# Performance work log

Hardware: AMD Instinct MI355X
Metric: run time of the kernel (lower is better)

The kernel has to match this reference:

```python
import jax, jax.numpy as jnp
import numpy as np

EPS = 1e-08


def setup_inputs() -> dict:
    key = jax.random.key(0)
    k1, k2, k3 = jax.random.split(key, 3)
    b, c, s = 4, 128, 32
    oc, k = 128, 3
    x = jax.random.normal(k1, (b, c, s, s, s), dtype=jnp.float32)
    y = jax.random.normal(k2, (b, c), dtype=jnp.float32)
    weight = jax.random.normal(k3, (oc, c, k, k, k), dtype=jnp.float32)
    return {"x": x, "y": y, "weight": weight}


def reference(x, y, weight):
    b, c, h, w, d = x.shape
    oc, ic, kh, kw, kd = weight.shape
    # modulate: per-sample scale of input channels
    ws = weight[None] * y[:, None, :, None, None, None]  # (b, oc, ic, k, k, k)
    # demodulate
    demod = jax.lax.rsqrt(jnp.sum(jnp.square(ws), axis=(2, 3, 4, 5)) + EPS)  # (b, oc)
    ws = ws * demod[:, :, None, None, None, None]
    # grouped conv: fold batch into channels, groups=b
    xr = x.reshape(1, b * c, h, w, d)
    wr = ws.reshape(b * oc, ic, kh, kw, kd)
    # same padding for stride=1, dilation=1: (k-1)//2
    pad = (kh - 1) // 2
    out = jax.lax.conv_general_dilated(
        xr, wr,
        window_strides=(1, 1, 1),
        padding=[(pad, pad)] * 3,
        feature_group_count=b,
        dimension_numbers=("NCDHW", "OIDHW", "NCDHW"),
    )
    return out.reshape(b, oc, h, w, d)
```

## Files before the change

### kernel.cpp

```cpp
#include <hip/hip_runtime.h>
#include <hip/hip_bf16.h>

typedef __attribute__((ext_vector_type(8))) short bf16x8;
typedef __attribute__((ext_vector_type(4))) float f32x4;
typedef unsigned short u16;
typedef unsigned int u32;

#define NP 34
#define XT_BYTES ((size_t)4 * NP * NP * NP * 128 * 2)

__device__ __forceinline__ u16 f2bf(float f) {
  __hip_bfloat16 h = __float2bfloat16(f);
  return __builtin_bit_cast(u16, h);
}

__device__ __forceinline__ void gload_lds16(const u16* g, u16* l) {
  __builtin_amdgcn_global_load_lds(
      (const __attribute__((address_space(1))) u32*)g,
      (__attribute__((address_space(3))) u32*)l, 16, 0, 0);
}

#define WAITV(N) asm volatile("s_waitcnt vmcnt(" #N ")" ::: "memory")
#define BAR() do { __builtin_amdgcn_s_barrier(); asm volatile("" ::: "memory"); } while (0)

__global__ __launch_bounds__(128) void kmodw(const float* __restrict__ w,
                                             const float* __restrict__ y,
                                             u16* __restrict__ wmod) {
  const int oc = blockIdx.x, b = blockIdx.y;
  const int ic = threadIdx.x;
  const float* wp = w + (oc * 128 + ic) * 27;
  float wv[27];
  float s = 0.f;
#pragma unroll
  for (int t = 0; t < 27; ++t) { wv[t] = wp[t]; s += wv[t] * wv[t]; }
  const float yv = y[b * 128 + ic];
  float v = yv * yv * s;
#pragma unroll
  for (int m = 1; m < 64; m <<= 1) v += __shfl_xor(v, m);
  __shared__ float part[2];
  const int lane = ic & 63, wid = ic >> 6;
  if (lane == 0) part[wid] = v;
  __syncthreads();
  const float demod = rsqrtf(part[0] + part[1] + 1e-8f);
  const float sc = yv * demod;
#pragma unroll
  for (int t = 0; t < 27; ++t)
    wmod[((b * 27 + t) * 128 + oc) * 128 + ic] = f2bf(wv[t] * sc);
}

__global__ __launch_bounds__(128) void khalo(u16* __restrict__ xt) {
  const int zy = blockIdx.x, b = blockIdx.y;
  const int zz = zy / NP, yy = zy % NP;
  u16* row = xt + ((size_t)((b * NP + zz) * NP + yy) * NP) * 128;
  u32* wp = (u32*)row;
  if (zz == 0 || zz == NP - 1 || yy == 0 || yy == NP - 1) {
#pragma unroll
    for (int i = 0; i < 17; ++i) wp[i * 128 + threadIdx.x] = 0;
  } else {
    if (threadIdx.x < 64) wp[threadIdx.x] = 0;
    else ((u32*)(row + 33 * 128))[threadIdx.x - 64] = 0;
  }
}

__global__ __launch_bounds__(256) void kcastx(const float* __restrict__ x,
                                              u16* __restrict__ xt) {
  const int yq = blockIdx.x, z = blockIdx.y, b = blockIdx.z;
  const int tid = threadIdx.x;
  __shared__ u16 t[32 * 132];
  const float* xp = x + (size_t)b * 128 * 32768 + (z * 32 + yq) * 32;
#pragma unroll
  for (int p = 0; p < 16; ++p) {
    const int ic = p * 8 + (tid >> 5), xx = tid & 31;
    t[xx * 132 + ic] = f2bf(xp[(size_t)ic * 32768 + xx]);
  }
  __syncthreads();
  u16* xtb = xt + (((size_t)(b * NP + z + 1) * NP + (yq + 1)) * NP + 1) * 128;
#pragma unroll
  for (int p = 0; p < 4; ++p) {
    const int xx = p * 8 + (tid >> 5), icq = tid & 31;
    *(ushort4*)(xtb + (size_t)xx * 128 + icq * 4) = *(const ushort4*)&t[xx * 132 + icq * 4];
  }
}

__global__ __launch_bounds__(512, 2) void kconv(const u16* __restrict__ xt,
                                                const u16* __restrict__ wmod,
                                                float* __restrict__ out) {
  __shared__ __align__(16) u16 Bsm[40960];
  __shared__ __align__(16) u16 Asm[3][8192];
  const int tid = threadIdx.x;
  const int lane = tid & 63, wn = tid >> 6;
  const int l15 = lane & 15, sgq = lane >> 4;
  const int bid = blockIdx.x;
  const int wgid = ((bid & 7) << 5) + (bid >> 3);
  const int b = wgid >> 6, yt = (wgid >> 5) & 1, z = wgid & 31;
  const int y0 = yt << 4;

  const u16* xb = xt + (size_t)b * (NP * NP * NP) * 128;
  const u16* wb = wmod + (size_t)b * 27 * 16384;

  f32x4 acc[8][4];
#pragma unroll
  for (int i = 0; i < 8; ++i)
#pragma unroll
    for (int j = 0; j < 4; ++j) acc[i][j] = (f32x4){0.f, 0.f, 0.f, 0.f};

  const int aoc = tid >> 3, aj = tid & 7;
  const u16* asrc = wb + (aoc << 7) + ((aj ^ (aoc & 7)) << 3);
  const int adst = tid << 3;

  int sybase[4], xp0[4];
#pragma unroll
  for (int nf = 0; nf < 4; ++nf) {
    sybase[nf] = (((wn << 1) + (nf >> 1)) + 1) * 2176;
    xp0[nf] = ((nf & 1) << 4) + l15 + 1;
  }
  const int kswz0 = sgq ^ (l15 & 7);

  auto stageA1 = [&](int ks2, int k) {
    const int g2 = ks2 / 9, j2 = ks2 - g2 * 9;
    const int tap = (g2 >> 1) * 9 + j2, hh = g2 & 1;
    gload_lds16(asrc + tap * 16384 + (hh << 6) + (k << 13),
                &Asm[ks2 % 3][adst + (k << 12)]);
  };
  auto stageB = [&](int g) {
    const int dz = (g >> 1) - 1, hh = g & 1;
    const int zrow = (z + 1 + dz) * NP + y0;
#pragma unroll
    for (int r = 0; r < 10; ++r) {
      int s = r * 512 + tid;
      const int dst = s << 3;
      s = s < 4896 ? s : 4895;
      const int sy = s / 272;
      const int rem = s - sy * 272;
      const int xpos = rem >> 3, j = rem & 7;
      gload_lds16(xb + (size_t)((zrow + sy) * NP + xpos) * 128 + (hh << 6) +
                      ((j ^ (xpos & 7)) << 3),
                  &Bsm[dst]);
    }
  };
  auto ldAf = [&](bf16x8* af, int par, int mh, int kswz) {
    const u16* Ah = &Asm[par][0];
#pragma unroll
    for (int mm = 0; mm < 4; ++mm) {
      const int oc = (mh << 6) + (mm << 4) + l15;
      af[mm] = *(const bf16x8*)&Ah[(oc << 6) + (kswz << 3)];
    }
  };
  auto ldBv = [&](bf16x8* bv, int kk, int dy, int dx) {
#pragma unroll
    for (int nf = 0; nf < 4; ++nf) {
      const int xp = xp0[nf] + dx;
      const int off = sybase[nf] + dy * 2176 + (xp << 6) +
                      ((((kk << 2) + sgq) ^ (xp & 7)) << 3);
      bv[nf] = *(const bf16x8*)&Bsm[off];
    }
  };

  bf16x8 af0[4], af1[4], bv0[4], bv1[4];

#define MFMA16(MH, AF, BV)                                                 \
  { __builtin_amdgcn_s_setprio(1);                                         \
    _Pragma("unroll") for (int mm = 0; mm < 4; ++mm)                       \
      _Pragma("unroll") for (int nf = 0; nf < 4; ++nf)                     \
        acc[(MH) * 4 + mm][nf] = __builtin_amdgcn_mfma_f32_16x16x32_bf16(  \
            (AF)[mm], (BV)[nf], acc[(MH) * 4 + mm][nf], 0, 0, 0);          \
    __builtin_amdgcn_s_setprio(0); }

  stageB(0);
  stageA1(0, 0); stageA1(0, 1);
  stageA1(1, 0); stageA1(1, 1);
  WAITV(0); BAR();

  for (int g = 0; g < 6; ++g) {
    for (int j = 0; j < 9; ++j) {
      const int ks = g * 9 + j;
      const int par = ks % 3;
      const int dy = j / 3 - 1, dx = (j % 3) - 1;
      const int ks2 = (ks + 2 <= 53) ? ks + 2 : 53;
      ldAf(af0, par, 0, kswz0);
      ldBv(bv0, 0, dy, dx);
      stageA1(ks2, 0);
      MFMA16(0, af0, bv0);
      ldAf(af1, par, 1, kswz0);
      stageA1(ks2, 1);
      MFMA16(1, af1, bv0);
      ldAf(af0, par, 0, kswz0 ^ 4);
      ldBv(bv1, 1, dy, dx);
      MFMA16(0, af0, bv1);
      ldAf(af1, par, 1, kswz0 ^ 4);
      MFMA16(1, af1, bv1);
      if (j < 8) {
        WAITV(2); BAR();
      } else if (g < 5) {
        BAR();
        stageB(g + 1);
        WAITV(0); BAR();
      }
    }
  }

#pragma unroll
  for (int m = 0; m < 8; ++m) {
    const int ocb = (m << 4) + (sgq << 2);
#pragma unroll
    for (int nf = 0; nf < 4; ++nf) {
      const int n = (wn << 6) + (nf << 4) + l15;
      const int yy = n >> 5, xx = n & 31;
      float* op = out + ((size_t)(b * 128 + ocb) << 15) + (z << 10) +
                  ((y0 + yy) << 5) + xx;
#pragma unroll
      for (int r = 0; r < 4; ++r) op[(size_t)r << 15] = acc[m][nf][r];
    }
  }
#undef MFMA16
}

extern "C" void kernel_launch(void* const* d_in, const int* in_sizes, int n_in,
                              void* d_out, int out_size, void* d_ws, size_t ws_size,
                              hipStream_t stream) {
  const float* x = (const float*)d_in[0];
  const float* y = (const float*)d_in[1];
  const float* w = (const float*)d_in[2];
  float* out = (float*)d_out;
  u16* xt = (u16*)d_ws;
  u16* wmod = (u16*)((char*)d_ws + XT_BYTES);

  hipLaunchKernelGGL(khalo, dim3(NP * NP, 4), dim3(128), 0, stream, xt);
  hipLaunchKernelGGL(kmodw, dim3(128, 4), dim3(128), 0, stream, w, y, wmod);
  hipLaunchKernelGGL(kcastx, dim3(32, 32, 4), dim3(256), 0, stream, x, xt);
  hipLaunchKernelGGL(kconv, dim3(256), dim3(512), 0, stream, xt, wmod, out);
}
```

Baseline: 122.8 us.

## Halve conv workgroup tile to 8 rows, 256 threads, double-buffered weights

The conv kernel now uses 256-thread workgroups that each cover 8 output rows instead of 16, doubling the grid to 512 blocks. The input slab shrinks to 10 rows, and the weight tile becomes double-buffered, with a full 128x64 slice staged each k-step. The smaller LDS footprint lets two workgroups share a CU, so one can hide the other's barrier stalls. In exchange, weights are reloaded twice as often across the grid, the halo overhead per block rises, and prefetch depth drops from two steps to one with a full vmcnt(0) wait each step.

```diff
diff --git a/kernel.cpp b/kernel.cpp
--- a/kernel.cpp
+++ b/kernel.cpp
@@ -82,21 +82,21 @@
   }
 }
 
-__global__ __launch_bounds__(512, 2) void kconv(const u16* __restrict__ xt,
+__global__ __launch_bounds__(256, 2) void kconv(const u16* __restrict__ xt,
                                                 const u16* __restrict__ wmod,
                                                 float* __restrict__ out) {
-  __shared__ __align__(16) u16 Bsm[40960];
-  __shared__ __align__(16) u16 Asm[3][8192];
+  __shared__ __align__(16) u16 Asm[2][8192];
+  __shared__ __align__(16) u16 Bsm[22528];
   const int tid = threadIdx.x;
   const int lane = tid & 63, wn = tid >> 6;
   const int l15 = lane & 15, sgq = lane >> 4;
   const int bid = blockIdx.x;
-  const int wgid = ((bid & 7) << 5) + (bid >> 3);
-  const int b = wgid >> 6, yt = (wgid >> 5) & 1, z = wgid & 31;
-  const int y0 = yt << 4;
-
+  const int wgid = ((bid & 7) << 6) + (bid >> 3);
+  const int b = wgid >> 7, yt = (wgid >> 5) & 3, z = wgid & 31;
+  const int y0 = yt << 3;
+
+  const u16* wb = wmod + (size_t)b * 27 * 16384;
   const u16* xb = xt + (size_t)b * (NP * NP * NP) * 128;
-  const u16* wb = wmod + (size_t)b * 27 * 16384;
 
   f32x4 acc[8][4];
 #pragma unroll
@@ -104,10 +104,9 @@
 #pragma unroll
     for (int j = 0; j < 4; ++j) acc[i][j] = (f32x4){0.f, 0.f, 0.f, 0.f};
 
-  const int aoc = tid >> 3, aj = tid & 7;
-  const u16* asrc = wb + (aoc << 7) + ((aj ^ (aoc & 7)) << 3);
+  const int aoc0 = tid >> 3, aj = tid & 7;
+  const u16* asrc = wb + (aoc0 << 7) + ((aj ^ (aoc0 & 7)) << 3);
   const int adst = tid << 3;
-
   int sybase[4], xp0[4];
 #pragma unroll
   for (int nf = 0; nf < 4; ++nf) {
@@ -116,24 +115,27 @@
   }
   const int kswz0 = sgq ^ (l15 & 7);
 
-  auto stageA1 = [&](int ks2, int k) {
-    const int g2 = ks2 / 9, j2 = ks2 - g2 * 9;
-    const int tap = (g2 >> 1) * 9 + j2, hh = g2 & 1;
-    gload_lds16(asrc + tap * 16384 + (hh << 6) + (k << 13),
-                &Asm[ks2 % 3][adst + (k << 12)]);
+  auto stageA = [&](int ks1) {
+    const int g1 = ks1 / 9, j1 = ks1 - g1 * 9;
+    const int tap = (g1 >> 1) * 9 + j1, hh = g1 & 1;
+    const u16* base = asrc + tap * 16384 + (hh << 6);
+    u16* dst = &Asm[ks1 & 1][adst];
+#pragma unroll
+    for (int k = 0; k < 4; ++k)
+      gload_lds16(base + (k << 12), dst + (k << 11));
   };
   auto stageB = [&](int g) {
     const int dz = (g >> 1) - 1, hh = g & 1;
-    const int zrow = (z + 1 + dz) * NP + y0;
-#pragma unroll
-    for (int r = 0; r < 10; ++r) {
-      int s = r * 512 + tid;
+    const int zro = (z + 1 + dz) * NP + y0;
+#pragma unroll
+    for (int r = 0; r < 11; ++r) {
+      int s = r * 256 + tid;
       const int dst = s << 3;
-      s = s < 4896 ? s : 4895;
+      s = s < 2719 ? s : 2719;
       const int sy = s / 272;
       const int rem = s - sy * 272;
       const int xpos = rem >> 3, j = rem & 7;
-      gload_lds16(xb + (size_t)((zrow + sy) * NP + xpos) * 128 + (hh << 6) +
+      gload_lds16(xb + (size_t)((zro + sy) * NP + xpos) * 128 + (hh << 6) +
                       ((j ^ (xpos & 7)) << 3),
                   &Bsm[dst]);
     }
@@ -167,33 +169,32 @@
     __builtin_amdgcn_s_setprio(0); }
 
   stageB(0);
-  stageA1(0, 0); stageA1(0, 1);
-  stageA1(1, 0); stageA1(1, 1);
+  stageA(0);
   WAITV(0); BAR();
 
   for (int g = 0; g < 6; ++g) {
     for (int j = 0; j < 9; ++j) {
       const int ks = g * 9 + j;
-      const int par = ks % 3;
+      const int par = ks & 1;
       const int dy = j / 3 - 1, dx = (j % 3) - 1;
-      const int ks2 = (ks + 2 <= 53) ? ks + 2 : 53;
+      if (ks < 53) stageA(ks + 1);
       ldAf(af0, par, 0, kswz0);
       ldBv(bv0, 0, dy, dx);
-      stageA1(ks2, 0);
       MFMA16(0, af0, bv0);
       ldAf(af1, par, 1, kswz0);
-      stageA1(ks2, 1);
       MFMA16(1, af1, bv0);
       ldAf(af0, par, 0, kswz0 ^ 4);
       ldBv(bv1, 1, dy, dx);
       MFMA16(0, af0, bv1);
       ldAf(af1, par, 1, kswz0 ^ 4);
       MFMA16(1, af1, bv1);
-      if (j < 8) {
-        WAITV(2); BAR();
-      } else if (g < 5) {
-        BAR();
-        stageB(g + 1);
+      if (j == 8) {
+        if (g < 5) {
+          BAR();
+          stageB(g + 1);
+          WAITV(0); BAR();
+        }
+      } else {
         WAITV(0); BAR();
       }
     }
@@ -228,5 +229,5 @@
   hipLaunchKernelGGL(khalo, dim3(NP * NP, 4), dim3(128), 0, stream, xt);
   hipLaunchKernelGGL(kmodw, dim3(128, 4), dim3(128), 0, stream, w, y, wmod);
   hipLaunchKernelGGL(kcastx, dim3(32, 32, 4), dim3(256), 0, stream, x, xt);
-  hipLaunchKernelGGL(kconv, dim3(256), dim3(512), 0, stream, xt, wmod, out);
-}
+  hipLaunchKernelGGL(kconv, dim3(512), dim3(256), 0, stream, xt, wmod, out);
+}
```

Result: faster. 119.0 us (-3.1%).

## Shrink conv workgroups to 128 threads with 4-row tiles and 32-wide K chunks

Applied to the files above, without the earlier changes.

The implicit-GEMM conv kernel now launches 1024 workgroups of 128 threads, each covering 4 y-rows of one z-slice, instead of 256 workgroups of 512 threads covering 16 rows. The K loop is split into 12 groups (four 32-channel quarters times three dz taps), with smaller swizzled LDS tiles for weights and the input halo, and each wave holds all 128 output channels. The goal is more resident workgroups per CU and a smaller LDS footprint for better occupancy and latency hiding. In exchange, the input halo is re-read more often relative to the compute it feeds, and there are more barriers per unit of work.

```diff
diff --git a/kernel.cpp b/kernel.cpp
--- a/kernel.cpp
+++ b/kernel.cpp
@@ -82,21 +82,21 @@
   }
 }
 
-__global__ __launch_bounds__(512, 2) void kconv(const u16* __restrict__ xt,
+__global__ __launch_bounds__(128, 2) void kconv(const u16* __restrict__ xt,
                                                 const u16* __restrict__ wmod,
                                                 float* __restrict__ out) {
-  __shared__ __align__(16) u16 Bsm[40960];
-  __shared__ __align__(16) u16 Asm[3][8192];
+  __shared__ __align__(16) u16 Asm[3][4096];
+  __shared__ __align__(16) u16 Bsm[7168];
   const int tid = threadIdx.x;
   const int lane = tid & 63, wn = tid >> 6;
   const int l15 = lane & 15, sgq = lane >> 4;
   const int bid = blockIdx.x;
-  const int wgid = ((bid & 7) << 5) + (bid >> 3);
-  const int b = wgid >> 6, yt = (wgid >> 5) & 1, z = wgid & 31;
-  const int y0 = yt << 4;
-
+  const int wgid = ((bid & 7) << 7) + (bid >> 3);
+  const int b = wgid >> 8, yt = (wgid >> 5) & 7, z = wgid & 31;
+  const int y0 = yt << 2;
+
+  const u16* wb = wmod + (size_t)b * 27 * 16384;
   const u16* xb = xt + (size_t)b * (NP * NP * NP) * 128;
-  const u16* wb = wmod + (size_t)b * 27 * 16384;
 
   f32x4 acc[8][4];
 #pragma unroll
@@ -104,99 +104,92 @@
 #pragma unroll
     for (int j = 0; j < 4; ++j) acc[i][j] = (f32x4){0.f, 0.f, 0.f, 0.f};
 
-  const int aoc = tid >> 3, aj = tid & 7;
-  const u16* asrc = wb + (aoc << 7) + ((aj ^ (aoc & 7)) << 3);
-  const int adst = tid << 3;
-
-  int sybase[4], xp0[4];
+  const int arow0 = tid >> 2;
+  const int av0 = (arow0 ^ (arow0 >> 2)) & 3;
+  const int aoff0 = arow0 * 128 + (((tid & 3) ^ av0) << 3);
+  const int adst0 = tid << 3;
+  const int slA = sgq ^ ((l15 ^ (l15 >> 2)) & 3);
+  const int afb = l15 * 32 + (slA << 3);
+  int rb[4];
 #pragma unroll
   for (int nf = 0; nf < 4; ++nf) {
-    sybase[nf] = (((wn << 1) + (nf >> 1)) + 1) * 2176;
-    xp0[nf] = ((nf & 1) << 4) + l15 + 1;
-  }
-  const int kswz0 = sgq ^ (l15 & 7);
-
-  auto stageA1 = [&](int ks2, int k) {
-    const int g2 = ks2 / 9, j2 = ks2 - g2 * 9;
-    const int tap = (g2 >> 1) * 9 + j2, hh = g2 & 1;
-    gload_lds16(asrc + tap * 16384 + (hh << 6) + (k << 13),
-                &Asm[ks2 % 3][adst + (k << 12)]);
+    const int n = (wn << 6) + (nf << 4) + l15;
+    rb[nf] = ((n >> 5) + 1) * 34 + (n & 31) + 1;
+  }
+
+  auto stageA = [&](int tap, int q32, int par) {
+    const u16* src = wb + tap * 16384 + q32 + aoff0;
+    u16* dst = &Asm[par][adst0];
+#pragma unroll
+    for (int k = 0; k < 4; ++k)
+      gload_lds16(src + (k << 12), dst + (k << 10));
   };
-  auto stageB = [&](int g) {
-    const int dz = (g >> 1) - 1, hh = g & 1;
-    const int zrow = (z + 1 + dz) * NP + y0;
-#pragma unroll
-    for (int r = 0; r < 10; ++r) {
-      int s = r * 512 + tid;
+  auto stageB = [&](int q, int dzi) {
+    const int pz = z + dzi;
+#pragma unroll
+    for (int r7 = 0; r7 < 7; ++r7) {
+      int s = (r7 << 7) + tid;
       const int dst = s << 3;
-      s = s < 4896 ? s : 4895;
-      const int sy = s / 272;
-      const int rem = s - sy * 272;
-      const int xpos = rem >> 3, j = rem & 7;
-      gload_lds16(xb + (size_t)((zrow + sy) * NP + xpos) * 128 + (hh << 6) +
-                      ((j ^ (xpos & 7)) << 3),
+      s = s < 815 ? s : 815;
+      const int r = s >> 2, jj = s & 3;
+      const int sy = r / 34, x = r - sy * 34;
+      const int vr = (r ^ (r >> 2)) & 3;
+      gload_lds16(xb + ((size_t)(pz * NP + (y0 + sy)) * NP + x) * 128 +
+                      (q << 5) + ((jj ^ vr) << 3),
                   &Bsm[dst]);
     }
   };
-  auto ldAf = [&](bf16x8* af, int par, int mh, int kswz) {
-    const u16* Ah = &Asm[par][0];
-#pragma unroll
-    for (int mm = 0; mm < 4; ++mm) {
-      const int oc = (mh << 6) + (mm << 4) + l15;
-      af[mm] = *(const bf16x8*)&Ah[(oc << 6) + (kswz << 3)];
-    }
-  };
-  auto ldBv = [&](bf16x8* bv, int kk, int dy, int dx) {
-#pragma unroll
-    for (int nf = 0; nf < 4; ++nf) {
-      const int xp = xp0[nf] + dx;
-      const int off = sybase[nf] + dy * 2176 + (xp << 6) +
-                      ((((kk << 2) + sgq) ^ (xp & 7)) << 3);
-      bv[nf] = *(const bf16x8*)&Bsm[off];
-    }
-  };
-
-  bf16x8 af0[4], af1[4], bv0[4], bv1[4];
-
-#define MFMA16(MH, AF, BV)                                                 \
+
+  bf16x8 af[8], bv[4];
+
+#define LDAF(PAR)                                                          \
+  { const u16* Ah = &Asm[PAR][afb];                                        \
+    _Pragma("unroll") for (int m = 0; m < 8; ++m)                          \
+      af[m] = *(const bf16x8*)&Ah[m << 9]; }
+#define LDBV(D)                                                            \
+  { _Pragma("unroll") for (int nf = 0; nf < 4; ++nf) {                     \
+      const int row = rb[nf] + (D);                                        \
+      const int v = (row ^ (row >> 2)) & 3;                                \
+      bv[nf] = *(const bf16x8*)&Bsm[(row << 5) + ((sgq ^ v) << 3)]; } }
+#define MFMA32()                                                           \
   { __builtin_amdgcn_s_setprio(1);                                         \
-    _Pragma("unroll") for (int mm = 0; mm < 4; ++mm)                       \
+    _Pragma("unroll") for (int mm = 0; mm < 8; ++mm)                       \
       _Pragma("unroll") for (int nf = 0; nf < 4; ++nf)                     \
-        acc[(MH) * 4 + mm][nf] = __builtin_amdgcn_mfma_f32_16x16x32_bf16(  \
-            (AF)[mm], (BV)[nf], acc[(MH) * 4 + mm][nf], 0, 0, 0);          \
+        acc[mm][nf] = __builtin_amdgcn_mfma_f32_16x16x32_bf16(             \
+            af[mm], bv[nf], acc[mm][nf], 0, 0, 0);                         \
     __builtin_amdgcn_s_setprio(0); }
 
-  stageB(0);
-  stageA1(0, 0); stageA1(0, 1);
-  stageA1(1, 0); stageA1(1, 1);
+  stageB(0, 0);
+  stageA(0, 0, 0);
+  stageA(1, 0, 1);
   WAITV(0); BAR();
 
-  for (int g = 0; g < 6; ++g) {
+  int q32 = 0, dzi = 0;
+  for (int g = 0; g < 12; ++g) {
+    const int gn = g + 1;
+    const int qn = gn < 12 ? gn / 3 : 0;
+    const int dzn = gn < 12 ? gn - qn * 3 : 0;
+    const int qn32 = qn << 5;
+#pragma unroll
     for (int j = 0; j < 9; ++j) {
-      const int ks = g * 9 + j;
-      const int par = ks % 3;
-      const int dy = j / 3 - 1, dx = (j % 3) - 1;
-      const int ks2 = (ks + 2 <= 53) ? ks + 2 : 53;
-      ldAf(af0, par, 0, kswz0);
-      ldBv(bv0, 0, dy, dx);
-      stageA1(ks2, 0);
-      MFMA16(0, af0, bv0);
-      ldAf(af1, par, 1, kswz0);
-      stageA1(ks2, 1);
-      MFMA16(1, af1, bv0);
-      ldAf(af0, par, 0, kswz0 ^ 4);
-      ldBv(bv1, 1, dy, dx);
-      MFMA16(0, af0, bv1);
-      ldAf(af1, par, 1, kswz0 ^ 4);
-      MFMA16(1, af1, bv1);
+      if (j <= 6) {
+        stageA(dzi * 9 + j + 2, q32, (j + 2) % 3);
+      } else if (g < 11) {
+        stageA(dzn * 9 + (j - 7), qn32, (j + 2) % 3);
+      }
+      LDAF(j % 3);
+      LDBV((j / 3 - 1) * 34 + (j % 3 - 1));
+      MFMA32();
       if (j < 8) {
-        WAITV(2); BAR();
-      } else if (g < 5) {
+        if (j == 7 && g == 11) { WAITV(0); BAR(); }
+        else { WAITV(4); BAR(); }
+      } else if (g < 11) {
         BAR();
-        stageB(g + 1);
+        stageB(qn, dzn);
         WAITV(0); BAR();
       }
     }
+    q32 = qn32; dzi = dzn;
   }
 
 #pragma unroll
@@ -212,7 +205,9 @@
       for (int r = 0; r < 4; ++r) op[(size_t)r << 15] = acc[m][nf][r];
     }
   }
-#undef MFMA16
+#undef LDAF
+#undef LDBV
+#undef MFMA32
 }
 
 extern "C" void kernel_launch(void* const* d_in, const int* in_sizes, int n_in,
@@ -228,5 +223,5 @@
   hipLaunchKernelGGL(khalo, dim3(NP * NP, 4), dim3(128), 0, stream, xt);
   hipLaunchKernelGGL(kmodw, dim3(128, 4), dim3(128), 0, stream, w, y, wmod);
   hipLaunchKernelGGL(kcastx, dim3(32, 32, 4), dim3(256), 0, stream, x, xt);
-  hipLaunchKernelGGL(kconv, dim3(256), dim3(512), 0, stream, xt, wmod, out);
-}
+  hipLaunchKernelGGL(kconv, dim3(1024), dim3(128), 0, stream, xt, wmod, out);
+}
```

After: 197.3 us. 1.61x slower.
